# Performance work log

Hardware: AMD Instinct MI355X
Metric: run time of the kernel (lower is better)

The kernel has to match this reference:

```python
import jax, jax.numpy as jnp
import numpy as np

N_NODES = 20000
N_EDGES = 320000


def cheb_conv(x, row, col, W, b):
    """PyG ChebConv with normalization='sym', lambda_max=2.0 (default).
    Scaled Laplacian L~ = L - I = -D^{-1/2} A D^{-1/2} (diagonal cancels:
    get_laplacian diag +1 plus add_self_loops fill -1).
    Tx_0 = x, Tx_1 = L~ x, Tx_k = 2 L~ Tx_{k-1} - Tx_{k-2};
    out = sum_k Tx_k @ W_k + b.
    """
    N = x.shape[0]
    mask = (row != col).astype(x.dtype)  # remove_self_loops
    deg = jax.ops.segment_sum(mask, row, num_segments=N)
    dis = jnp.where(deg > 0, 1.0 / jnp.sqrt(deg), 0.0)  # deg_inv_sqrt, inf->0
    w = -dis[row] * dis[col] * mask  # edge weights of L~ (diag entries are 0)

    def prop(t):  # y = L~ t via gather-scale-scatter over edges
        return jax.ops.segment_sum(w[:, None] * t[col], row, num_segments=N)

    K = W.shape[0]
    Tx0 = x
    out = Tx0 @ W[0]
    Tx1 = prop(Tx0)
    if K > 1:
        out = out + Tx1 @ W[1]
    for k in range(2, K):
        Tx2 = 2.0 * prop(Tx1) - Tx0
        out = out + Tx2 @ W[k]
        Tx0, Tx1 = Tx1, Tx2
    return out + b


def setup_inputs() -> dict:
    key = jax.random.key(0)
    ks = jax.random.split(key, 10)
    x = jax.random.normal(ks[0], (N_NODES, 1152), dtype=jnp.float32)
    row = jax.random.randint(ks[1], (N_EDGES,), 0, N_NODES)
    col = jax.random.randint(ks[2], (N_EDGES,), 0, N_NODES)
    s1 = 1.0 / np.sqrt(1152)
    s2 = 1.0 / np.sqrt(1152)
    s3 = 1.0 / np.sqrt(576)
    W1 = jax.random.normal(ks[3], (6, 1152, 1152), dtype=jnp.float32) * s1
    b1 = jax.random.normal(ks[4], (1152,), dtype=jnp.float32) * 0.01
    W2 = jax.random.normal(ks[5], (5, 1152, 576), dtype=jnp.float32) * s2
    b2 = jax.random.normal(ks[6], (576,), dtype=jnp.float32) * 0.01
    W3 = jax.random.normal(ks[7], (5, 576, 288), dtype=jnp.float32) * s3
    b3 = jax.random.normal(ks[8], (288,), dtype=jnp.float32) * 0.01
    return {"x": x, "row": row, "col": col, "W1": W1, "b1": b1,
            "W2": W2, "b2": b2, "W3": W3, "b3": b3}


def reference(x, row, col, W1, b1, W2, b2, W3, b3):
    # dropout(0.1) is identity in eval mode
    h = jax.nn.relu(cheb_conv(x, row, col, W1, b1))
    h = jax.nn.relu(cheb_conv(h, row, col, W2, b2))
    h = jax.nn.relu(cheb_conv(h, row, col, W3, b3))
    return h
```

## Files before the change

kernel.cpp:

```cpp
#include <hip/hip_runtime.h>
#include <hip/hip_bf16.h>

#define N_NODES 20000
#define N_EDGES 320000

typedef __attribute__((ext_vector_type(8))) short shortx8;
typedef __attribute__((ext_vector_type(4))) float floatx4;
using bf16 = __hip_bfloat16;

typedef __attribute__((address_space(1))) const unsigned int GuT;
typedef __attribute__((address_space(3))) unsigned int LuT;
__device__ __forceinline__ void gl2lds16(const bf16* g, bf16* l) {
  __builtin_amdgcn_global_load_lds((GuT*)g, (LuT*)l, 16, 0, 0);
}

__device__ inline float b2f(unsigned short u) {
  union { unsigned int i; float f; } x;
  x.i = ((unsigned int)u) << 16;
  return x.f;
}
__device__ inline unsigned short f2b(float f) {
  bf16 h(f);
  return *(unsigned short*)&h;
}

struct APtrs { const bf16* p[6]; };


__global__ void zero_kernel(int* p, int n) {
  int i = blockIdx.x * 256 + threadIdx.x;
  if (i < n) p[i] = 0;
}

__global__ void deg_kernel(const int* __restrict__ row, const int* __restrict__ col,
                           int* __restrict__ deg, int nE) {
  int e = blockIdx.x * 256 + threadIdx.x;
  if (e >= nE) return;
  int r = row[e], c = col[e];
  if (r != c) atomicAdd(&deg[r], 1);
}

__global__ void dis_kernel(const int* __restrict__ deg, float* __restrict__ dis, int n) {
  int i = blockIdx.x * 256 + threadIdx.x;
  if (i >= n) return;
  int d = deg[i];
  dis[i] = (d > 0) ? (1.0f / sqrtf((float)d)) : 0.0f;
}

__global__ __launch_bounds__(1024) void scan_kernel(const int* __restrict__ deg,
                                                    int* __restrict__ row_ptr,
                                                    int* __restrict__ cursor, int n) {
  __shared__ int part[1024];
  int t = threadIdx.x;
  int base = t * 20;
  int loc[20];
  int s = 0;
#pragma unroll
  for (int i = 0; i < 20; i++) {
    int idx = base + i;
    int v = (idx < n) ? deg[idx] : 0;
    loc[i] = s;
    s += v;
  }
  part[t] = s;
  __syncthreads();
  for (int offd = 1; offd < 1024; offd <<= 1) {
    int v = (t >= offd) ? part[t - offd] : 0;
    __syncthreads();
    part[t] += v;
    __syncthreads();
  }
  int basev = (t > 0) ? part[t - 1] : 0;
#pragma unroll
  for (int i = 0; i < 20; i++) {
    int idx = base + i;
    if (idx < n) {
      int rp = basev + loc[i];
      row_ptr[idx] = rp;
      cursor[idx] = rp;
    }
  }
  if (t == 1023) row_ptr[n] = part[1023];
}

__global__ void scatter_kernel(const int* __restrict__ row, const int* __restrict__ col,
                               const float* __restrict__ dis, int* __restrict__ cursor,
                               int* __restrict__ col_s, float* __restrict__ w_s, int nE) {
  int e = blockIdx.x * 256 + threadIdx.x;
  if (e >= nE) return;
  int r = row[e], c = col[e];
  if (r == c) return;
  int p = atomicAdd(&cursor[r], 1);
  col_s[p] = c;
  w_s[p] = -dis[r] * dis[c];
}


__global__ void wtrans_kernel(const float* __restrict__ W, bf16* __restrict__ Wt,
                              int K_, int I, int J) {
  __shared__ float tile[32][33];
  int jt = blockIdx.x % (J / 32);
  int rest = blockIdx.x / (J / 32);
  int it = rest % (I / 32);
  int k = rest / (I / 32);
  int tx = threadIdx.x, ty = threadIdx.y;
  const float* src = W + (size_t)k * I * J;
  for (int r = ty; r < 32; r += 8)
    tile[r][tx] = src[(size_t)(it * 32 + r) * J + jt * 32 + tx];
  __syncthreads();
  for (int r = ty; r < 32; r += 8) {
    int j = jt * 32 + r;
    Wt[((size_t)k * J + j) * I + it * 32 + tx] = bf16(tile[tx][r]);
  }
}


__global__ void cast_x_kernel(const float* __restrict__ x, bf16* __restrict__ dst, int n4) {
  int idx = blockIdx.x * 256 + threadIdx.x;
  if (idx >= n4) return;
  int flat = idx * 4;
  float4 v = *(const float4*)(x + flat);
  dst[flat + 0] = bf16(v.x);
  dst[flat + 1] = bf16(v.y);
  dst[flat + 2] = bf16(v.z);
  dst[flat + 3] = bf16(v.w);
}


template <int F, int VEC>
__global__ __launch_bounds__(320) void prop_kernel(
    const int* __restrict__ row_ptr, const int* __restrict__ col_s,
    const float* __restrict__ w_s, const bf16* __restrict__ src,
    const bf16* tx0, bf16* dst) {
  constexpr int C = F / VEC;
  int node = blockIdx.x;
  int t = threadIdx.x;
  bool act = t < C;
  int fb = t * VEC;
  int e0 = row_ptr[node], e1 = row_ptr[node + 1];
  float acc[VEC];
#pragma unroll
  for (int q = 0; q < VEC; q++) acc[q] = 0.0f;

  const unsigned short* sp = (const unsigned short*)src;
  int e = e0;
  for (; e + 16 <= e1; e += 16) {
    int cs[16];
    float wv[16];
#pragma unroll
    for (int u = 0; u < 16; u++) {
      cs[u] = col_s[e + u];
      wv[u] = w_s[e + u];
    }
    if (act) {
      if constexpr (VEC == 4) {
        ushort4 v[16];
#pragma unroll
        for (int u = 0; u < 16; u++) v[u] = *(const ushort4*)(sp + (size_t)cs[u] * F + fb);
#pragma unroll
        for (int u = 0; u < 16; u++) {
          acc[0] += wv[u] * b2f(v[u].x);
          acc[1] += wv[u] * b2f(v[u].y);
          acc[2] += wv[u] * b2f(v[u].z);
          acc[3] += wv[u] * b2f(v[u].w);
        }
      } else {
        ushort2 v[16];
#pragma unroll
        for (int u = 0; u < 16; u++) v[u] = *(const ushort2*)(sp + (size_t)cs[u] * F + fb);
#pragma unroll
        for (int u = 0; u < 16; u++) {
          acc[0] += wv[u] * b2f(v[u].x);
          acc[1] += wv[u] * b2f(v[u].y);
        }
      }
    }
  }
  for (; e + 4 <= e1; e += 4) {
    int cs[4];
    float wv[4];
#pragma unroll
    for (int u = 0; u < 4; u++) {
      cs[u] = col_s[e + u];
      wv[u] = w_s[e + u];
    }
    if (act) {
      if constexpr (VEC == 4) {
        ushort4 v[4];
#pragma unroll
        for (int u = 0; u < 4; u++) v[u] = *(const ushort4*)(sp + (size_t)cs[u] * F + fb);
#pragma unroll
        for (int u = 0; u < 4; u++) {
          acc[0] += wv[u] * b2f(v[u].x);
          acc[1] += wv[u] * b2f(v[u].y);
          acc[2] += wv[u] * b2f(v[u].z);
          acc[3] += wv[u] * b2f(v[u].w);
        }
      } else {
        ushort2 v[4];
#pragma unroll
        for (int u = 0; u < 4; u++) v[u] = *(const ushort2*)(sp + (size_t)cs[u] * F + fb);
#pragma unroll
        for (int u = 0; u < 4; u++) {
          acc[0] += wv[u] * b2f(v[u].x);
          acc[1] += wv[u] * b2f(v[u].y);
        }
      }
    }
  }
  for (; e < e1; e++) {
    int c = col_s[e];
    float w = w_s[e];
    if (act) {
      if constexpr (VEC == 4) {
        ushort4 v = *(const ushort4*)(sp + (size_t)c * F + fb);
        acc[0] += w * b2f(v.x);
        acc[1] += w * b2f(v.y);
        acc[2] += w * b2f(v.z);
        acc[3] += w * b2f(v.w);
      } else {
        ushort2 v = *(const ushort2*)(sp + (size_t)c * F + fb);
        acc[0] += w * b2f(v.x);
        acc[1] += w * b2f(v.y);
      }
    }
  }

  if (!act) return;
  unsigned short* dp = (unsigned short*)dst + (size_t)node * F + fb;
  if (tx0) {
    const unsigned short* t0 = (const unsigned short*)tx0 + (size_t)node * F + fb;
    if constexpr (VEC == 4) {
      ushort4 tv = *(const ushort4*)t0;
      ushort4 o;
      o.x = f2b(2.0f * acc[0] - b2f(tv.x));
      o.y = f2b(2.0f * acc[1] - b2f(tv.y));
      o.z = f2b(2.0f * acc[2] - b2f(tv.z));
      o.w = f2b(2.0f * acc[3] - b2f(tv.w));
      *(ushort4*)dp = o;
    } else {
      ushort2 tv = *(const ushort2*)t0;
      ushort2 o;
      o.x = f2b(2.0f * acc[0] - b2f(tv.x));
      o.y = f2b(2.0f * acc[1] - b2f(tv.y));
      *(ushort2*)dp = o;
    }
  } else {
    if constexpr (VEC == 4) {
      ushort4 o;
      o.x = f2b(acc[0]);
      o.y = f2b(acc[1]);
      o.z = f2b(acc[2]);
      o.w = f2b(acc[3]);
      *(ushort4*)dp = o;
    } else {
      ushort2 o;
      o.x = f2b(acc[0]);
      o.y = f2b(acc[1]);
      *(ushort2*)dp = o;
    }
  }
}


template <int MODE, int NSEG>
__global__ __launch_bounds__(256) void gemm_kernel(
    APtrs ap, const bf16* __restrict__ Bbase,
    const float* __restrict__ bias, float* __restrict__ accbuf,
    void* __restrict__ dst, int M, int Nout, int Kt, int dstLd) {
  __shared__ bf16 As[128 * 32];
  __shared__ bf16 Bs[128 * 32];
  int nb = (Nout + 127) >> 7;
  int mtiles = (M + 127) >> 7;
  int xcd = blockIdx.x & 7;
  int s = blockIdx.x >> 3;
  int bn = s % nb;
  int bm = (s / nb) * 8 + xcd;
  if (bm >= mtiles) return;
  int m0 = bm << 7, n0 = bn << 7;
  int t = threadIdx.x;
  int lane = t & 63;
  int wave = t >> 6;
  int wm = wave & 1, wn = wave >> 1;
  int l16 = lane & 15;
  int k8 = (lane >> 4) << 3;
  floatx4 acc[4][4] = {};

  int srow = lane >> 2;
  int scol = (lane & 3) << 3;

#pragma unroll
  for (int seg = 0; seg < NSEG; seg++) {
    const bf16* A = ap.p[seg];
    const bf16* Bt = Bbase + (size_t)seg * Nout * Kt;
#pragma unroll 1
    for (int kt = 0; kt < Kt; kt += 32) {
#pragma unroll
      for (int q = 0; q < 2; q++) {
        int inst = (wave << 1) + q;
        int r = (inst << 4) + srow;
        int ga = m0 + r;
        if (ga < M)
          gl2lds16(A + (size_t)ga * Kt + kt + scol, &As[inst << 9]);
        int gb = n0 + r;
        if (gb < Nout)
          gl2lds16(Bt + (size_t)gb * Kt + kt + scol, &Bs[inst << 9]);
      }
      __syncthreads();
      shortx8 af[4], bfr[4];
#pragma unroll
      for (int i = 0; i < 4; i++)
        af[i] = *(const shortx8*)&As[(((wm << 6) + (i << 4) + l16) << 5) + k8];
#pragma unroll
      for (int j = 0; j < 4; j++)
        bfr[j] = *(const shortx8*)&Bs[(((wn << 6) + (j << 4) + l16) << 5) + k8];
#pragma unroll
      for (int i = 0; i < 4; i++)
#pragma unroll
        for (int j = 0; j < 4; j++)
          acc[i][j] = __builtin_amdgcn_mfma_f32_16x16x32_bf16(af[i], bfr[j], acc[i][j], 0, 0, 0);
      __syncthreads();
    }
  }

  int lq = lane >> 4;
#pragma unroll
  for (int j = 0; j < 4; j++) {
    int colg = n0 + (wn << 6) + (j << 4) + l16;
    if (colg >= Nout) continue;
    float bv = (MODE == 0 || MODE == 4 || MODE == 5) ? bias[colg] : 0.0f;
#pragma unroll
    for (int i = 0; i < 4; i++) {
      int rowb = m0 + (wm << 6) + (i << 4) + (lq << 2);
#pragma unroll
      for (int q = 0; q < 4; q++) {
        int rowg = rowb + q;
        if (rowg >= M) continue;
        float v = acc[i][j][q];
        size_t aidx = (size_t)rowg * Nout + colg;
        if constexpr (MODE == 0) {
          accbuf[aidx] = v + bv;
        } else if constexpr (MODE == 1) {
          accbuf[aidx] += v;
        } else if constexpr (MODE == 2) {
          float s2 = fmaxf(accbuf[aidx] + v, 0.0f);
          ((bf16*)dst)[(size_t)rowg * dstLd + colg] = bf16(s2);
        } else if constexpr (MODE == 3) {
          float s2 = fmaxf(accbuf[aidx] + v, 0.0f);
          ((float*)dst)[(size_t)rowg * Nout + colg] = s2;
        } else if constexpr (MODE == 4) {
          float s2 = fmaxf(v + bv, 0.0f);
          ((bf16*)dst)[(size_t)rowg * dstLd + colg] = bf16(s2);
        } else {
          float s2 = fmaxf(v + bv, 0.0f);
          ((float*)dst)[(size_t)rowg * Nout + colg] = s2;
        }
      }
    }
  }
}


extern "C" void kernel_launch(void* const* d_in, const int* in_sizes, int n_in,
                              void* d_out, int out_size, void* d_ws, size_t ws_size,
                              hipStream_t stream) {
  const float* x = (const float*)d_in[0];
  const int* row = (const int*)d_in[1];
  const int* col = (const int*)d_in[2];
  const float* W1 = (const float*)d_in[3];
  const float* b1 = (const float*)d_in[4];
  const float* W2 = (const float*)d_in[5];
  const float* b2 = (const float*)d_in[6];
  const float* W3 = (const float*)d_in[7];
  const float* b3 = (const float*)d_in[8];

  char* ws = (char*)d_ws;
  size_t off = 0;
  auto alloc = [&](size_t bytes) -> void* {
    void* p = ws + off;
    off += (bytes + 255) & ~(size_t)255;
    return p;
  };

  const size_t TXB = (size_t)N_NODES * 1152 * 2;
  bf16* Wt = (bf16*)alloc((size_t)6 * 1152 * 1152 * 2);
  int* deg = (int*)alloc(N_NODES * 4);
  float* dis = (float*)alloc(N_NODES * 4);
  int* row_ptr = (int*)alloc((N_NODES + 1) * 4);
  int* cursor = (int*)alloc(N_NODES * 4);
  int* col_s = (int*)alloc(N_EDGES * 4);
  float* w_s = (float*)alloc(N_EDGES * 4);
  size_t off_common = off;

  size_t need_A = off_common + 7 * ((TXB + 255) & ~(size_t)255);
  size_t need_B = off_common + 3 * ((TXB + 255) & ~(size_t)255) +
                  (((size_t)N_NODES * 1152 * 4 + 255) & ~(size_t)255);
  int tier = (ws_size >= need_A) ? 0 : (ws_size >= need_B) ? 1 : 2;

  zero_kernel<<<(N_NODES + 255) / 256, 256, 0, stream>>>(deg, N_NODES);
  deg_kernel<<<(N_EDGES + 255) / 256, 256, 0, stream>>>(row, col, deg, N_EDGES);
  dis_kernel<<<(N_NODES + 255) / 256, 256, 0, stream>>>(deg, dis, N_NODES);
  scan_kernel<<<1, 1024, 0, stream>>>(deg, row_ptr, cursor, N_NODES);
  scatter_kernel<<<(N_EDGES + 255) / 256, 256, 0, stream>>>(row, col, dis, cursor,
                                                            col_s, w_s, N_EDGES);

  const int MT = (N_NODES + 127) >> 7;
  const int GMT = 8 * ((MT + 7) >> 3);
  const bf16* NB = nullptr;
  const int NX = N_NODES * 1152 / 4;

  if (tier == 0) {
    bf16* T[7];
    for (int i = 0; i < 7; i++) T[i] = (bf16*)alloc(TXB);

    wtrans_kernel<<<6 * 36 * 36, dim3(32, 8), 0, stream>>>(W1, Wt, 6, 1152, 1152);
    cast_x_kernel<<<(NX + 255) / 256, 256, 0, stream>>>(x, T[0], NX);
    prop_kernel<1152, 4><<<N_NODES, 320, 0, stream>>>(row_ptr, col_s, w_s, T[0], NB, T[1]);
    prop_kernel<1152, 4><<<N_NODES, 320, 0, stream>>>(row_ptr, col_s, w_s, T[1], T[0], T[2]);
    prop_kernel<1152, 4><<<N_NODES, 320, 0, stream>>>(row_ptr, col_s, w_s, T[2], T[1], T[3]);
    prop_kernel<1152, 4><<<N_NODES, 320, 0, stream>>>(row_ptr, col_s, w_s, T[3], T[2], T[4]);
    prop_kernel<1152, 4><<<N_NODES, 320, 0, stream>>>(row_ptr, col_s, w_s, T[4], T[3], T[5]);
    {
      APtrs a = {{T[0], T[1], T[2], T[3], T[4], T[5]}};
      gemm_kernel<4, 6><<<GMT * 9, 256, 0, stream>>>(a, Wt, b1, nullptr, T[6],
                                                     N_NODES, 1152, 1152, 1152);
    }

    wtrans_kernel<<<5 * 36 * 18, dim3(32, 8), 0, stream>>>(W2, Wt, 5, 1152, 576);
    prop_kernel<1152, 4><<<N_NODES, 320, 0, stream>>>(row_ptr, col_s, w_s, T[6], NB, T[0]);
    prop_kernel<1152, 4><<<N_NODES, 320, 0, stream>>>(row_ptr, col_s, w_s, T[0], T[6], T[1]);
    prop_kernel<1152, 4><<<N_NODES, 320, 0, stream>>>(row_ptr, col_s, w_s, T[1], T[0], T[2]);
    prop_kernel<1152, 4><<<N_NODES, 320, 0, stream>>>(row_ptr, col_s, w_s, T[2], T[1], T[3]);
    {
      APtrs a = {{T[6], T[0], T[1], T[2], T[3], nullptr}};
      gemm_kernel<4, 5><<<GMT * 5, 256, 0, stream>>>(a, Wt, b2, nullptr, T[4],
                                                     N_NODES, 576, 1152, 576);
    }

    wtrans_kernel<<<5 * 18 * 9, dim3(32, 8), 0, stream>>>(W3, Wt, 5, 576, 288);
    prop_kernel<576, 2><<<N_NODES, 320, 0, stream>>>(row_ptr, col_s, w_s, T[4], NB, T[5]);
    prop_kernel<576, 2><<<N_NODES, 320, 0, stream>>>(row_ptr, col_s, w_s, T[5], T[4], T[0]);
    prop_kernel<576, 2><<<N_NODES, 320, 0, stream>>>(row_ptr, col_s, w_s, T[0], T[5], T[1]);
    prop_kernel<576, 2><<<N_NODES, 320, 0, stream>>>(row_ptr, col_s, w_s, T[1], T[0], T[2]);
    {
      APtrs a = {{T[4], T[5], T[0], T[1], T[2], nullptr}};
      gemm_kernel<5, 5><<<GMT * 3, 256, 0, stream>>>(a, Wt, b3, nullptr, d_out,
                                                     N_NODES, 288, 576, 0);
    }
    return;
  }

  bf16* TxP = (bf16*)alloc(TXB);
  bf16* TxQ = (bf16*)alloc(TXB);
  bf16* Th = (tier == 1) ? (bf16*)alloc(TXB) : nullptr;
  float* accb = (float*)alloc((size_t)N_NODES * 1152 * 4);
  if (off > ws_size) return;

  wtrans_kernel<<<6 * 36 * 36, dim3(32, 8), 0, stream>>>(W1, Wt, 6, 1152, 1152);
  cast_x_kernel<<<(NX + 255) / 256, 256, 0, stream>>>(x, TxP, NX);
  {
    const int F = 1152, NO = 1152, nb = 9;
    size_t wsl = (size_t)NO * F;
    prop_kernel<1152, 4><<<N_NODES, 320, 0, stream>>>(row_ptr, col_s, w_s, TxP, NB, TxQ);
    APtrs a01 = {{TxP, TxQ}};
    gemm_kernel<0, 2><<<GMT * nb, 256, 0, stream>>>(a01, Wt, b1, accb, nullptr,
                                                    N_NODES, NO, F, 0);
    prop_kernel<1152, 4><<<N_NODES, 320, 0, stream>>>(row_ptr, col_s, w_s, TxQ, TxP, TxP);
    prop_kernel<1152, 4><<<N_NODES, 320, 0, stream>>>(row_ptr, col_s, w_s, TxP, TxQ, TxQ);
    APtrs a23 = {{TxP, TxQ}};
    gemm_kernel<1, 2><<<GMT * nb, 256, 0, stream>>>(a23, Wt + 2 * wsl, b1, accb, nullptr,
                                                    N_NODES, NO, F, 0);
    prop_kernel<1152, 4><<<N_NODES, 320, 0, stream>>>(row_ptr, col_s, w_s, TxQ, TxP, TxP);
    prop_kernel<1152, 4><<<N_NODES, 320, 0, stream>>>(row_ptr, col_s, w_s, TxP, TxQ, TxQ);
    if (tier == 1) {
      APtrs a45 = {{TxP, TxQ}};
      gemm_kernel<2, 2><<<GMT * nb, 256, 0, stream>>>(a45, Wt + 4 * wsl, b1, accb, Th,
                                                      N_NODES, NO, F, 1152);
    } else {
      APtrs a4 = {{TxP}};
      gemm_kernel<1, 1><<<GMT * nb, 256, 0, stream>>>(a4, Wt + 4 * wsl, b1, accb, nullptr,
                                                      N_NODES, NO, F, 0);
      APtrs a5 = {{TxQ}};
      gemm_kernel<2, 1><<<GMT * nb, 256, 0, stream>>>(a5, Wt + 5 * wsl, b1, accb, TxP,
                                                      N_NODES, NO, F, 1152);
    }
  }

  bf16* h1 = (tier == 1) ? Th : TxP;
  bf16* u0 = (tier == 1) ? TxP : TxQ;
  bf16* u1 = (tier == 1) ? TxQ : TxP;

  wtrans_kernel<<<5 * 36 * 18, dim3(32, 8), 0, stream>>>(W2, Wt, 5, 1152, 576);
  {
    const int F = 1152, NO = 576, nb = 5;
    size_t wsl = (size_t)NO * F;
    prop_kernel<1152, 4><<<N_NODES, 320, 0, stream>>>(row_ptr, col_s, w_s, h1, NB, u0);
    APtrs a01 = {{h1, u0}};
    gemm_kernel<0, 2><<<GMT * nb, 256, 0, stream>>>(a01, Wt, b2, accb, nullptr,
                                                    N_NODES, NO, F, 0);
    prop_kernel<1152, 4><<<N_NODES, 320, 0, stream>>>(row_ptr, col_s, w_s, u0, h1, h1);
    prop_kernel<1152, 4><<<N_NODES, 320, 0, stream>>>(row_ptr, col_s, w_s, h1, u0, u0);
    APtrs a23 = {{h1, u0}};
    gemm_kernel<1, 2><<<GMT * nb, 256, 0, stream>>>(a23, Wt + 2 * wsl, b2, accb, nullptr,
                                                    N_NODES, NO, F, 0);
    prop_kernel<1152, 4><<<N_NODES, 320, 0, stream>>>(row_ptr, col_s, w_s, u0, h1, h1);
    APtrs a4 = {{h1}};
    gemm_kernel<2, 1><<<GMT * nb, 256, 0, stream>>>(a4, Wt + 4 * wsl, b2, accb, u0,
                                                    N_NODES, NO, F, 576);
  }

  bf16* h2 = u0;

  wtrans_kernel<<<5 * 18 * 9, dim3(32, 8), 0, stream>>>(W3, Wt, 5, 576, 288);
  {
    const int F = 576, NO = 288, nb = 3;
    size_t wsl = (size_t)NO * F;
    prop_kernel<576, 2><<<N_NODES, 320, 0, stream>>>(row_ptr, col_s, w_s, h2, NB, u1);
    APtrs a01 = {{h2, u1}};
    gemm_kernel<0, 2><<<GMT * nb, 256, 0, stream>>>(a01, Wt, b3, accb, nullptr,
                                                    N_NODES, NO, F, 0);
    prop_kernel<576, 2><<<N_NODES, 320, 0, stream>>>(row_ptr, col_s, w_s, u1, h2, h2);
    prop_kernel<576, 2><<<N_NODES, 320, 0, stream>>>(row_ptr, col_s, w_s, h2, u1, u1);
    APtrs a23 = {{h2, u1}};
    gemm_kernel<1, 2><<<GMT * nb, 256, 0, stream>>>(a23, Wt + 2 * wsl, b3, accb, nullptr,
                                                    N_NODES, NO, F, 0);
    prop_kernel<576, 2><<<N_NODES, 320, 0, stream>>>(row_ptr, col_s, w_s, u1, h2, h2);
    APtrs a4 = {{h2}};
    gemm_kernel<3, 1><<<GMT * nb, 256, 0, stream>>>(a4, Wt + 4 * wsl, b3, accb, d_out,
                                                    N_NODES, NO, F, 0);
  }
}
```

Before: 2.136 ms.

## Slice feature dimension in 1152-wide propagation for better gather cache locality

Adds a prop_slice_kernel that handles each node with one wave and a 96-column feature slice, four nodes per block. The 1152 features are covered by two launches, one for columns 0–767 and one for 768–1151, so each launch gathers from a narrower part of the source matrix and should get better cache reuse across the random neighbor reads. Output stores and Tx0 loads use nontemporal hints. It also drops the VEC=4 path from prop_kernel. The cost is lanes 48–63 of every wave sitting idle, plus the edge list being read once per slice.

```diff
diff --git a/kernel.cpp b/kernel.cpp
--- a/kernel.cpp
+++ b/kernel.cpp
@@ -127,6 +127,90 @@
 }
 
 
+template <int LOGC>
+__global__ __launch_bounds__(256) void prop_slice_kernel(
+    const int* __restrict__ row_ptr, const int* __restrict__ col_s,
+    const float* __restrict__ w_s, const bf16* __restrict__ src,
+    const bf16* tx0, bf16* dst, int fbase) {
+  constexpr int CH = 1 << LOGC;
+  int g = blockIdx.x >> LOGC;
+  int c = blockIdx.x & (CH - 1);
+  int wave = threadIdx.x >> 6;
+  int lane = threadIdx.x & 63;
+  int node = g * 4 + wave;
+  bool act = lane < 48;
+  int fb = fbase + c * 96 + lane * 2;
+  int e0 = row_ptr[node], e1 = row_ptr[node + 1];
+  float a0 = 0.0f, a1 = 0.0f;
+  const unsigned short* sp = (const unsigned short*)src;
+
+  int e = e0;
+  for (; e + 16 <= e1; e += 16) {
+    int cs[16];
+    float wv[16];
+#pragma unroll
+    for (int u = 0; u < 16; u++) {
+      cs[u] = col_s[e + u];
+      wv[u] = w_s[e + u];
+    }
+    if (act) {
+      ushort2 v[16];
+#pragma unroll
+      for (int u = 0; u < 16; u++) v[u] = *(const ushort2*)(sp + (size_t)cs[u] * 1152 + fb);
+#pragma unroll
+      for (int u = 0; u < 16; u++) {
+        a0 += wv[u] * b2f(v[u].x);
+        a1 += wv[u] * b2f(v[u].y);
+      }
+    }
+  }
+  for (; e + 4 <= e1; e += 4) {
+    int cs[4];
+    float wv[4];
+#pragma unroll
+    for (int u = 0; u < 4; u++) {
+      cs[u] = col_s[e + u];
+      wv[u] = w_s[e + u];
+    }
+    if (act) {
+      ushort2 v[4];
+#pragma unroll
+      for (int u = 0; u < 4; u++) v[u] = *(const ushort2*)(sp + (size_t)cs[u] * 1152 + fb);
+#pragma unroll
+      for (int u = 0; u < 4; u++) {
+        a0 += wv[u] * b2f(v[u].x);
+        a1 += wv[u] * b2f(v[u].y);
+      }
+    }
+  }
+  for (; e < e1; e++) {
+    int cc = col_s[e];
+    float w = w_s[e];
+    if (act) {
+      ushort2 v = *(const ushort2*)(sp + (size_t)cc * 1152 + fb);
+      a0 += w * b2f(v.x);
+      a1 += w * b2f(v.y);
+    }
+  }
+
+  if (!act) return;
+  unsigned int* dp = (unsigned int*)((unsigned short*)dst + (size_t)node * 1152 + fb);
+  ushort2 o;
+  if (tx0) {
+    const unsigned int* t0 =
+        (const unsigned int*)((const unsigned short*)tx0 + (size_t)node * 1152 + fb);
+    unsigned int tvu = __builtin_nontemporal_load(t0);
+    ushort2 tv = *(ushort2*)&tvu;
+    o.x = f2b(2.0f * a0 - b2f(tv.x));
+    o.y = f2b(2.0f * a1 - b2f(tv.y));
+  } else {
+    o.x = f2b(a0);
+    o.y = f2b(a1);
+  }
+  __builtin_nontemporal_store(*(unsigned int*)&o, dp);
+}
+
+
 template <int F, int VEC>
 __global__ __launch_bounds__(320) void prop_kernel(
     const int* __restrict__ row_ptr, const int* __restrict__ col_s,
@@ -153,26 +237,13 @@
       wv[u] = w_s[e + u];
     }
     if (act) {
-      if constexpr (VEC == 4) {
-        ushort4 v[16];
-#pragma unroll
-        for (int u = 0; u < 16; u++) v[u] = *(const ushort4*)(sp + (size_t)cs[u] * F + fb);
-#pragma unroll
-        for (int u = 0; u < 16; u++) {
-          acc[0] += wv[u] * b2f(v[u].x);
-          acc[1] += wv[u] * b2f(v[u].y);
-          acc[2] += wv[u] * b2f(v[u].z);
-          acc[3] += wv[u] * b2f(v[u].w);
-        }
-      } else {
-        ushort2 v[16];
-#pragma unroll
-        for (int u = 0; u < 16; u++) v[u] = *(const ushort2*)(sp + (size_t)cs[u] * F + fb);
-#pragma unroll
-        for (int u = 0; u < 16; u++) {
-          acc[0] += wv[u] * b2f(v[u].x);
-          acc[1] += wv[u] * b2f(v[u].y);
-        }
+      ushort2 v[16];
+#pragma unroll
+      for (int u = 0; u < 16; u++) v[u] = *(const ushort2*)(sp + (size_t)cs[u] * F + fb);
+#pragma unroll
+      for (int u = 0; u < 16; u++) {
+        acc[0] += wv[u] * b2f(v[u].x);
+        acc[1] += wv[u] * b2f(v[u].y);
       }
     }
   }
@@ -185,26 +256,13 @@
       wv[u] = w_s[e + u];
     }
     if (act) {
-      if constexpr (VEC == 4) {
-        ushort4 v[4];
-#pragma unroll
-        for (int u = 0; u < 4; u++) v[u] = *(const ushort4*)(sp + (size_t)cs[u] * F + fb);
-#pragma unroll
-        for (int u = 0; u < 4; u++) {
-          acc[0] += wv[u] * b2f(v[u].x);
-          acc[1] += wv[u] * b2f(v[u].y);
-          acc[2] += wv[u] * b2f(v[u].z);
-          acc[3] += wv[u] * b2f(v[u].w);
-        }
-      } else {
-        ushort2 v[4];
-#pragma unroll
-        for (int u = 0; u < 4; u++) v[u] = *(const ushort2*)(sp + (size_t)cs[u] * F + fb);
-#pragma unroll
-        for (int u = 0; u < 4; u++) {
-          acc[0] += wv[u] * b2f(v[u].x);
-          acc[1] += wv[u] * b2f(v[u].y);
-        }
+      ushort2 v[4];
+#pragma unroll
+      for (int u = 0; u < 4; u++) v[u] = *(const ushort2*)(sp + (size_t)cs[u] * F + fb);
+#pragma unroll
+      for (int u = 0; u < 4; u++) {
+        acc[0] += wv[u] * b2f(v[u].x);
+        acc[1] += wv[u] * b2f(v[u].y);
       }
     }
   }
@@ -212,17 +270,9 @@
     int c = col_s[e];
     float w = w_s[e];
     if (act) {
-      if constexpr (VEC == 4) {
-        ushort4 v = *(const ushort4*)(sp + (size_t)c * F + fb);
-        acc[0] += w * b2f(v.x);
-        acc[1] += w * b2f(v.y);
-        acc[2] += w * b2f(v.z);
-        acc[3] += w * b2f(v.w);
-      } else {
-        ushort2 v = *(const ushort2*)(sp + (size_t)c * F + fb);
-        acc[0] += w * b2f(v.x);
-        acc[1] += w * b2f(v.y);
-      }
+      ushort2 v = *(const ushort2*)(sp + (size_t)c * F + fb);
+      acc[0] += w * b2f(v.x);
+      acc[1] += w * b2f(v.y);
     }
   }
 
@@ -230,35 +280,16 @@
   unsigned short* dp = (unsigned short*)dst + (size_t)node * F + fb;
   if (tx0) {
     const unsigned short* t0 = (const unsigned short*)tx0 + (size_t)node * F + fb;
-    if constexpr (VEC == 4) {
-      ushort4 tv = *(const ushort4*)t0;
-      ushort4 o;
-      o.x = f2b(2.0f * acc[0] - b2f(tv.x));
-      o.y = f2b(2.0f * acc[1] - b2f(tv.y));
-      o.z = f2b(2.0f * acc[2] - b2f(tv.z));
-      o.w = f2b(2.0f * acc[3] - b2f(tv.w));
-      *(ushort4*)dp = o;
-    } else {
-      ushort2 tv = *(const ushort2*)t0;
-      ushort2 o;
-      o.x = f2b(2.0f * acc[0] - b2f(tv.x));
-      o.y = f2b(2.0f * acc[1] - b2f(tv.y));
-      *(ushort2*)dp = o;
-    }
+    ushort2 tv = *(const ushort2*)t0;
+    ushort2 o;
+    o.x = f2b(2.0f * acc[0] - b2f(tv.x));
+    o.y = f2b(2.0f * acc[1] - b2f(tv.y));
+    *(ushort2*)dp = o;
   } else {
-    if constexpr (VEC == 4) {
-      ushort4 o;
-      o.x = f2b(acc[0]);
-      o.y = f2b(acc[1]);
-      o.z = f2b(acc[2]);
-      o.w = f2b(acc[3]);
-      *(ushort4*)dp = o;
-    } else {
-      ushort2 o;
-      o.x = f2b(acc[0]);
-      o.y = f2b(acc[1]);
-      *(ushort2*)dp = o;
-    }
+    ushort2 o;
+    o.x = f2b(acc[0]);
+    o.y = f2b(acc[1]);
+    *(ushort2*)dp = o;
   }
 }
 
@@ -409,17 +440,24 @@
   const bf16* NB = nullptr;
   const int NX = N_NODES * 1152 / 4;
 
+  auto prop1152 = [&](const bf16* src, const bf16* tx0, bf16* dst) {
+    prop_slice_kernel<3><<<(N_NODES / 4) * 8, 256, 0, stream>>>(row_ptr, col_s, w_s,
+                                                                src, tx0, dst, 0);
+    prop_slice_kernel<2><<<(N_NODES / 4) * 4, 256, 0, stream>>>(row_ptr, col_s, w_s,
+                                                                src, tx0, dst, 768);
+  };
+
   if (tier == 0) {
     bf16* T[7];
     for (int i = 0; i < 7; i++) T[i] = (bf16*)alloc(TXB);
 
     wtrans_kernel<<<6 * 36 * 36, dim3(32, 8), 0, stream>>>(W1, Wt, 6, 1152, 1152);
     cast_x_kernel<<<(NX + 255) / 256, 256, 0, stream>>>(x, T[0], NX);
-    prop_kernel<1152, 4><<<N_NODES, 320, 0, stream>>>(row_ptr, col_s, w_s, T[0], NB, T[1]);
-    prop_kernel<1152, 4><<<N_NODES, 320, 0, stream>>>(row_ptr, col_s, w_s, T[1], T[0], T[2]);
-    prop_kernel<1152, 4><<<N_NODES, 320, 0, stream>>>(row_ptr, col_s, w_s, T[2], T[1], T[3]);
-    prop_kernel<1152, 4><<<N_NODES, 320, 0, stream>>>(row_ptr, col_s, w_s, T[3], T[2], T[4]);
-    prop_kernel<1152, 4><<<N_NODES, 320, 0, stream>>>(row_ptr, col_s, w_s, T[4], T[3], T[5]);
+    prop1152(T[0], NB, T[1]);
+    prop1152(T[1], T[0], T[2]);
+    prop1152(T[2], T[1], T[3]);
+    prop1152(T[3], T[2], T[4]);
+    prop1152(T[4], T[3], T[5]);
     {
       APtrs a = {{T[0], T[1], T[2], T[3], T[4], T[5]}};
       gemm_kernel<4, 6><<<GMT * 9, 256, 0, stream>>>(a, Wt, b1, nullptr, T[6],
@@ -427,10 +465,10 @@
     }
 
     wtrans_kernel<<<5 * 36 * 18, dim3(32, 8), 0, stream>>>(W2, Wt, 5, 1152, 576);
-    prop_kernel<1152, 4><<<N_NODES, 320, 0, stream>>>(row_ptr, col_s, w_s, T[6], NB, T[0]);
-    prop_kernel<1152, 4><<<N_NODES, 320, 0, stream>>>(row_ptr, col_s, w_s, T[0], T[6], T[1]);
-    prop_kernel<1152, 4><<<N_NODES, 320, 0, stream>>>(row_ptr, col_s, w_s, T[1], T[0], T[2]);
-    prop_kernel<1152, 4><<<N_NODES, 320, 0, stream>>>(row_ptr, col_s, w_s, T[2], T[1], T[3]);
+    prop1152(T[6], NB, T[0]);
+    prop1152(T[0], T[6], T[1]);
+    prop1152(T[1], T[0], T[2]);
+    prop1152(T[2], T[1], T[3]);
     {
       APtrs a = {{T[6], T[0], T[1], T[2], T[3], nullptr}};
       gemm_kernel<4, 5><<<GMT * 5, 256, 0, stream>>>(a, Wt, b2, nullptr, T[4],
@@ -461,17 +499,17 @@
   {
     const int F = 1152, NO = 1152, nb = 9;
     size_t wsl = (size_t)NO * F;
-    prop_kernel<1152, 4><<<N_NODES, 320, 0, stream>>>(row_ptr, col_s, w_s, TxP, NB, TxQ);
+    prop1152(TxP, NB, TxQ);
     APtrs a01 = {{TxP, TxQ}};
     gemm_kernel<0, 2><<<GMT * nb, 256, 0, stream>>>(a01, Wt, b1, accb, nullptr,
                                                     N_NODES, NO, F, 0);
-    prop_kernel<1152, 4><<<N_NODES, 320, 0, stream>>>(row_ptr, col_s, w_s, TxQ, TxP, TxP);
-    prop_kernel<1152, 4><<<N_NODES, 320, 0, stream>>>(row_ptr, col_s, w_s, TxP, TxQ, TxQ);
+    prop1152(TxQ, TxP, TxP);
+    prop1152(TxP, TxQ, TxQ);
     APtrs a23 = {{TxP, TxQ}};
     gemm_kernel<1, 2><<<GMT * nb, 256, 0, stream>>>(a23, Wt + 2 * wsl, b1, accb, nullptr,
                                                     N_NODES, NO, F, 0);
-    prop_kernel<1152, 4><<<N_NODES, 320, 0, stream>>>(row_ptr, col_s, w_s, TxQ, TxP, TxP);
-    prop_kernel<1152, 4><<<N_NODES, 320, 0, stream>>>(row_ptr, col_s, w_s, TxP, TxQ, TxQ);
+    prop1152(TxQ, TxP, TxP);
+    prop1152(TxP, TxQ, TxQ);
     if (tier == 1) {
       APtrs a45 = {{TxP, TxQ}};
       gemm_kernel<2, 2><<<GMT * nb, 256, 0, stream>>>(a45, Wt + 4 * wsl, b1, accb, Th,
@@ -494,16 +532,16 @@
   {
     const int F = 1152, NO = 576, nb = 5;
     size_t wsl = (size_t)NO * F;
-    prop_kernel<1152, 4><<<N_NODES, 320, 0, stream>>>(row_ptr, col_s, w_s, h1, NB, u0);
+    prop1152(h1, NB, u0);
     APtrs a01 = {{h1, u0}};
     gemm_kernel<0, 2><<<GMT * nb, 256, 0, stream>>>(a01, Wt, b2, accb, nullptr,
                                                     N_NODES, NO, F, 0);
-    prop_kernel<1152, 4><<<N_NODES, 320, 0, stream>>>(row_ptr, col_s, w_s, u0, h1, h1);
-    prop_kernel<1152, 4><<<N_NODES, 320, 0, stream>>>(row_ptr, col_s, w_s, h1, u0, u0);
+    prop1152(u0, h1, h1);
+    prop1152(h1, u0, u0);
     APtrs a23 = {{h1, u0}};
     gemm_kernel<1, 2><<<GMT * nb, 256, 0, stream>>>(a23, Wt + 2 * wsl, b2, accb, nullptr,
                                                     N_NODES, NO, F, 0);
-    prop_kernel<1152, 4><<<N_NODES, 320, 0, stream>>>(row_ptr, col_s, w_s, u0, h1, h1);
+    prop1152(u0, h1, h1);
     APtrs a4 = {{h1}};
     gemm_kernel<2, 1><<<GMT * nb, 256, 0, stream>>>(a4, Wt + 4 * wsl, b2, accb, u0,
                                                     N_NODES, NO, F, 576);
```

Result: slower. 2.759 ms (+29.2%).
